# Kernel tuning notes

Measured on AMD Instinct MI355X. Metric: run time of the kernel, lower is better.

## Reference

```python
import jax, jax.numpy as jnp
import numpy as np

NUM_IN = 1024
HIDDEN = 32  # pooling_hidden_dim fixed in PoolingFunction
N = 200000


def setup_inputs() -> dict:
    key = jax.random.key(0)
    ks = jax.random.split(key, 7)
    s_in = 1.0 / np.sqrt(NUM_IN)
    s_h = 1.0 / np.sqrt(HIDDEN)
    return {
        "x": jax.random.normal(ks[0], (N, NUM_IN), dtype=jnp.float32),
        "V_w": jax.random.uniform(ks[1], (HIDDEN, NUM_IN), jnp.float32, -s_in, s_in),
        "V_b": jax.random.uniform(ks[2], (HIDDEN,), jnp.float32, -s_in, s_in),
        "U_w": jax.random.uniform(ks[3], (HIDDEN, NUM_IN), jnp.float32, -s_in, s_in),
        "U_b": jax.random.uniform(ks[4], (HIDDEN,), jnp.float32, -s_in, s_in),
        "w_w": jax.random.uniform(ks[5], (1, HIDDEN), jnp.float32, -s_h, s_h),
        "w_b": jax.random.uniform(ks[6], (1,), jnp.float32, -s_h, s_h),
    }


def reference(x, V_w, V_b, U_w, U_b, w_w, w_b):
    # x: [N, num_in]
    a_v = jnp.tanh(x @ V_w.T + V_b)          # [N, H]
    a_u = jax.nn.sigmoid(x @ U_w.T + U_b)    # [N, H]
    a = (a_v * a_u) @ w_w.T + w_b            # [N, 1] attention logits
    a = jax.nn.softmax(a.T, axis=1)          # [1, N]
    m = a @ x                                # [1, num_in]
    return m
```

## Files before the change

kernel.cpp:

```cpp
#include <hip/hip_runtime.h>
#include <math.h>

#define NUM_IN 1024
#define TILE_R 16
#define NB_MAX 256
#define PR_OSTRIDE 17
#define PR_QSTRIDE (64 * PR_OSTRIDE + 4)

using bf16x8 = __attribute__((ext_vector_type(8))) short;
using f32x4  = __attribute__((ext_vector_type(4))) float;

__device__ __forceinline__ unsigned int f2bf1(float f) {
  unsigned int u = __float_as_uint(f);
  return (u + 0x7fffu + ((u >> 16) & 1u)) >> 16;
}
__device__ __forceinline__ unsigned int pk2(float a, float b) {
  return f2bf1(a) | (f2bf1(b) << 16);
}
__device__ __forceinline__ float bflo(unsigned int w) { return __uint_as_float(w << 16); }
__device__ __forceinline__ float bfhi(unsigned int w) { return __uint_as_float(w & 0xffff0000u); }

#define BARX() do { \
  __builtin_amdgcn_sched_barrier(0); \
  asm volatile("s_waitcnt lgkmcnt(0)" ::: "memory"); \
  __builtin_amdgcn_s_barrier(); \
  __builtin_amdgcn_sched_barrier(0); \
} while (0)

#define WAIT_VM0() do { \
  __builtin_amdgcn_sched_barrier(0); \
  asm volatile("s_waitcnt vmcnt(0)" ::: "memory"); \
  __builtin_amdgcn_sched_barrier(0); \
} while (0)

__global__ __launch_bounds__(512, 1) void ga_main(
    const float* __restrict__ x,
    const float* __restrict__ Vw, const float* __restrict__ Uw,
    const float* __restrict__ Vb, const float* __restrict__ Ub,
    const float* __restrict__ ww, const float* __restrict__ wb,
    float* __restrict__ wsAcc, float* __restrict__ wsM, float* __restrict__ wsS,
    int nb, int nTiles)
{
  __shared__ __align__(16) float prered[8 * PR_QSTRIDE];
  __shared__ __align__(16) float lgs[TILE_R];

  const int tid = threadIdx.x;
  const int b   = blockIdx.x;
  const int w   = tid >> 6;
  const int l   = tid & 63;
  const int l15 = l & 15;
  const int kg  = l >> 4;
  const int h   = tid & 31;
  const int rr  = tid >> 5;

  const float vbh = Vb[h], ubh = Ub[h], wwh = ww[h];
  const float wb0 = wb[0];

  uint4 bfr[4][4];
  {
    #pragma unroll
    for (int nt = 0; nt < 4; ++nt) {
      const int o = (nt << 4) + l15;
      const float* Wr = (o < 32) ? (Vw + (size_t)o * NUM_IN) : (Uw + (size_t)(o - 32) * NUM_IN);
      #pragma unroll
      for (int s = 0; s < 4; ++s) {
        const int k0 = (w << 7) + (s << 5) + (kg << 3);
        const float4 a = *reinterpret_cast<const float4*>(Wr + k0);
        const float4 c = *reinterpret_cast<const float4*>(Wr + k0 + 4);
        uint4 v;
        v.x = pk2(a.x, a.y); v.y = pk2(a.z, a.w);
        v.z = pk2(c.x, c.y); v.w = pk2(c.z, c.w);
        bfr[nt][s] = v;
      }
    }
    #pragma unroll
    for (int nt = 0; nt < 4; ++nt)
      #pragma unroll
      for (int s = 0; s < 4; ++s)
        asm volatile("" : "+v"(bfr[nt][s].x), "+v"(bfr[nt][s].y),
                          "+v"(bfr[nt][s].z), "+v"(bfr[nt][s].w));
  }

  const char* xb8 = (const char*)x;
  const int inRow = (w << 9) + (kg << 5);

  float4 sA[4], sB[4];
  uint4  xf[4];

  #define ISSUE(Tt) do { \
    const char* base_ = xb8 + ((size_t)(Tt) * TILE_R + l15) * 4096 + inRow; \
    sA[0] = *reinterpret_cast<const float4*>(base_      );  sB[0] = *reinterpret_cast<const float4*>(base_ +  16); \
    sA[1] = *reinterpret_cast<const float4*>(base_ + 128);  sB[1] = *reinterpret_cast<const float4*>(base_ + 144); \
    sA[2] = *reinterpret_cast<const float4*>(base_ + 256);  sB[2] = *reinterpret_cast<const float4*>(base_ + 272); \
    sA[3] = *reinterpret_cast<const float4*>(base_ + 384);  sB[3] = *reinterpret_cast<const float4*>(base_ + 400); \
  } while (0)

  #define PACK() do { \
    _Pragma("unroll") \
    for (int s = 0; s < 4; ++s) { \
      xf[s].x = pk2(sA[s].x, sA[s].y); xf[s].y = pk2(sA[s].z, sA[s].w); \
      xf[s].z = pk2(sB[s].x, sB[s].y); xf[s].w = pk2(sB[s].z, sB[s].w); \
    } \
    _Pragma("unroll") \
    for (int s = 0; s < 4; ++s) \
      asm volatile("" : "+v"(xf[s].x), "+v"(xf[s].y), "+v"(xf[s].z), "+v"(xf[s].w)); \
  } while (0)

  float M = -INFINITY, S = 0.f;
  float acc[4][8];
  #pragma unroll
  for (int s = 0; s < 4; ++s)
    #pragma unroll
    for (int i = 0; i < 8; ++i) acc[s][i] = 0.f;

  int T = b;

  ISSUE(T);
  WAIT_VM0();
  PACK();
  if (T + nb < nTiles) ISSUE(T + nb);

  while (true) {
    const bool more1 = (T + nb)     < nTiles;
    const bool more2 = (T + 2 * nb) < nTiles;

    {
      f32x4 a4[4] = {{0.f,0.f,0.f,0.f},{0.f,0.f,0.f,0.f},{0.f,0.f,0.f,0.f},{0.f,0.f,0.f,0.f}};
      #pragma unroll
      for (int s = 0; s < 4; ++s) {
        const bf16x8 af = __builtin_bit_cast(bf16x8, xf[s]);
        #pragma unroll
        for (int nt = 0; nt < 4; ++nt)
          a4[nt] = __builtin_amdgcn_mfma_f32_16x16x32_bf16(
              af, __builtin_bit_cast(bf16x8, bfr[nt][s]), a4[nt], 0, 0, 0);
      }
      #pragma unroll
      for (int nt = 0; nt < 4; ++nt) {
        const int obase = w * PR_QSTRIDE + ((nt << 4) + l15) * PR_OSTRIDE + (kg << 2);
        #pragma unroll
        for (int r = 0; r < 4; ++r) prered[obase + r] = a4[nt][r];
      }
    }
    BARX();

    {
      float pv = vbh, pu = ubh;
      #pragma unroll
      for (int q = 0; q < 8; ++q) {
        pv += prered[q * PR_QSTRIDE + h * PR_OSTRIDE + rr];
        pu += prered[q * PR_QSTRIDE + (h + 32) * PR_OSTRIDE + rr];
      }
      const float ev = __expf(2.f * pv);
      const float av = (ev - 1.f) * __builtin_amdgcn_rcpf(ev + 1.f);
      const float au = __builtin_amdgcn_rcpf(1.f + __expf(-pu));
      float g = av * au * wwh;
      g += __shfl_xor(g, 1);
      g += __shfl_xor(g, 2);
      g += __shfl_xor(g, 4);
      g += __shfl_xor(g, 8);
      g += __shfl_xor(g, 16);
      if (h == 0) lgs[rr] = g + wb0;
    }
    BARX();

    {
      const float lf = lgs[l15];
      float mc = lf;
      mc = fmaxf(mc, __shfl_xor(mc, 1));
      mc = fmaxf(mc, __shfl_xor(mc, 2));
      mc = fmaxf(mc, __shfl_xor(mc, 4));
      mc = fmaxf(mc, __shfl_xor(mc, 8));
      if (mc > M) {
        const float scale = __expf(M - mc);
        S *= scale;
        #pragma unroll
        for (int s = 0; s < 4; ++s)
          #pragma unroll
          for (int i = 0; i < 8; ++i) acc[s][i] *= scale;
        M = mc;
      }
      const float p = __expf(lf - M);
      S += p;
      #pragma unroll
      for (int s = 0; s < 4; ++s) {
        acc[s][0] = fmaf(p, bflo(xf[s].x), acc[s][0]);
        acc[s][1] = fmaf(p, bfhi(xf[s].x), acc[s][1]);
        acc[s][2] = fmaf(p, bflo(xf[s].y), acc[s][2]);
        acc[s][3] = fmaf(p, bfhi(xf[s].y), acc[s][3]);
        acc[s][4] = fmaf(p, bflo(xf[s].z), acc[s][4]);
        acc[s][5] = fmaf(p, bfhi(xf[s].z), acc[s][5]);
        acc[s][6] = fmaf(p, bflo(xf[s].w), acc[s][6]);
        acc[s][7] = fmaf(p, bfhi(xf[s].w), acc[s][7]);
      }
      if (more1) {
        WAIT_VM0();
        PACK();
        if (more2) ISSUE(T + 2 * nb);
      }
    }

    if (!more1) break;
    T += nb;
  }

  #pragma unroll
  for (int d = 1; d < 16; d <<= 1) {
    #pragma unroll
    for (int s = 0; s < 4; ++s)
      #pragma unroll
      for (int i = 0; i < 8; ++i) acc[s][i] += __shfl_xor(acc[s][i], d);
    S += __shfl_xor(S, d);
  }
  if (l15 == 0) {
    #pragma unroll
    for (int s = 0; s < 4; ++s) {
      float* dst = &wsAcc[(size_t)b * NUM_IN + (w << 7) + (s << 5) + (kg << 3)];
      *reinterpret_cast<float4*>(dst)     = make_float4(acc[s][0], acc[s][1], acc[s][2], acc[s][3]);
      *reinterpret_cast<float4*>(dst + 4) = make_float4(acc[s][4], acc[s][5], acc[s][6], acc[s][7]);
    }
  }
  if (tid == 0) { wsM[b] = M; wsS[b] = S; }
}

__global__ void ga_reduceMS(const float* __restrict__ wsM, const float* __restrict__ wsS,
                            float* __restrict__ wsW, float* __restrict__ wsT, int nb)
{
  __shared__ float sm[8], ss[8];
  const int t = threadIdx.x;
  float m = (t < nb) ? wsM[t] : -INFINITY;
  float mm = m;
  #pragma unroll
  for (int d = 1; d < 64; d <<= 1) mm = fmaxf(mm, __shfl_xor(mm, d));
  if ((t & 63) == 0) sm[t >> 6] = mm;
  __syncthreads();
  const float M = fmaxf(fmaxf(fmaxf(sm[0], sm[1]), fmaxf(sm[2], sm[3])),
                        fmaxf(fmaxf(sm[4], sm[5]), fmaxf(sm[6], sm[7])));
  const float wg = (t < nb) ? __expf(m - M) : 0.f;
  if (t < nb) wsW[t] = wg;
  float s = wg * ((t < nb) ? wsS[t] : 0.f);
  #pragma unroll
  for (int d = 1; d < 64; d <<= 1) s += __shfl_xor(s, d);
  if ((t & 63) == 0) ss[t >> 6] = s;
  __syncthreads();
  if (t == 0) {
    float St = 0.f;
    #pragma unroll
    for (int k = 0; k < 8; ++k) St += ss[k];
    wsT[0] = St;
  }
}

__global__ void ga_combine(const float* __restrict__ wsAcc, const float* __restrict__ wsW,
                           const float* __restrict__ wsT, float* __restrict__ out, int nb)
{
  __shared__ float red[8][32];
  const int t = threadIdx.x;
  const int col = (blockIdx.x << 5) + (t & 31);
  const int seg = t >> 5;
  float s = 0.f;
  for (int ii = 0; ii < 64; ++ii) {
    const int i = (seg << 6) + ii;
    if (i < nb) s = fmaf(wsW[i], wsAcc[(size_t)i * NUM_IN + col], s);
  }
  red[seg][t & 31] = s;
  __syncthreads();
  if (seg == 0) {
    float tot = 0.f;
    #pragma unroll
    for (int k = 0; k < 8; ++k) tot += red[k][t];
    out[col] = tot / wsT[0];
  }
}

extern "C" void kernel_launch(void* const* d_in, const int* in_sizes, int n_in,
                              void* d_out, int out_size, void* d_ws, size_t ws_size,
                              hipStream_t stream)
{
  const float* x  = (const float*)d_in[0];
  const float* Vw = (const float*)d_in[1];
  const float* Vb = (const float*)d_in[2];
  const float* Uw = (const float*)d_in[3];
  const float* Ub = (const float*)d_in[4];
  const float* ww = (const float*)d_in[5];
  const float* wb = (const float*)d_in[6];
  float* out = (float*)d_out;

  const int Nrows  = in_sizes[0] / NUM_IN;
  const int nTiles = Nrows / TILE_R;

  const size_t per = (size_t)NUM_IN * 4 + 16;
  int nb = (int)((ws_size - 64) / per);
  if (nb > NB_MAX)  nb = NB_MAX;
  if (nb > nTiles)  nb = nTiles;
  if (nb < 1)       nb = 1;

  float* wsAcc = (float*)d_ws;
  float* wsM   = wsAcc + (size_t)nb * NUM_IN;
  float* wsS   = wsM + nb;
  float* wsW   = wsS + nb;
  float* wsT   = wsW + nb;

  ga_main<<<nb, 512, 0, stream>>>(x, Vw, Uw, Vb, Ub, ww, wb, wsAcc, wsM, wsS, nb, nTiles);
  ga_reduceMS<<<1, 512, 0, stream>>>(wsM, wsS, wsW, wsT, nb);
  ga_combine<<<32, 256, 0, stream>>>(wsAcc, wsW, wsT, out, nb);
}
```

Baseline: 180.5 us.

## Deepen x-tile prefetch to two in-flight loads with double register sets

```diff
diff --git a/kernel.cpp b/kernel.cpp
--- a/kernel.cpp
+++ b/kernel.cpp
@@ -27,9 +27,9 @@
   __builtin_amdgcn_sched_barrier(0); \
 } while (0)
 
-#define WAIT_VM0() do { \
+#define WAIT_VM(n) do { \
   __builtin_amdgcn_sched_barrier(0); \
-  asm volatile("s_waitcnt vmcnt(0)" ::: "memory"); \
+  asm volatile("s_waitcnt vmcnt(" #n ")" ::: "memory"); \
   __builtin_amdgcn_sched_barrier(0); \
 } while (0)
 
@@ -84,22 +84,23 @@
   const char* xb8 = (const char*)x;
   const int inRow = (w << 9) + (kg << 5);
 
-  float4 sA[4], sB[4];
+  float4 sA0[4], sB0[4], sA1[4], sB1[4];
   uint4  xf[4];
 
-  #define ISSUE(Tt) do { \
-    const char* base_ = xb8 + ((size_t)(Tt) * TILE_R + l15) * 4096 + inRow; \
-    sA[0] = *reinterpret_cast<const float4*>(base_      );  sB[0] = *reinterpret_cast<const float4*>(base_ +  16); \
-    sA[1] = *reinterpret_cast<const float4*>(base_ + 128);  sB[1] = *reinterpret_cast<const float4*>(base_ + 144); \
-    sA[2] = *reinterpret_cast<const float4*>(base_ + 256);  sB[2] = *reinterpret_cast<const float4*>(base_ + 272); \
-    sA[3] = *reinterpret_cast<const float4*>(base_ + 384);  sB[3] = *reinterpret_cast<const float4*>(base_ + 400); \
+  #define ISSUE_SET(sa, sb, Tt) do { \
+    const int Tc_ = ((Tt) < nTiles) ? (Tt) : (nTiles - 1); \
+    const char* base_ = xb8 + ((size_t)Tc_ * TILE_R + l15) * 4096 + inRow; \
+    sa[0] = *reinterpret_cast<const float4*>(base_      );  sb[0] = *reinterpret_cast<const float4*>(base_ +  16); \
+    sa[1] = *reinterpret_cast<const float4*>(base_ + 128);  sb[1] = *reinterpret_cast<const float4*>(base_ + 144); \
+    sa[2] = *reinterpret_cast<const float4*>(base_ + 256);  sb[2] = *reinterpret_cast<const float4*>(base_ + 272); \
+    sa[3] = *reinterpret_cast<const float4*>(base_ + 384);  sb[3] = *reinterpret_cast<const float4*>(base_ + 400); \
   } while (0)
 
-  #define PACK() do { \
+  #define PACK_SET(sa, sb) do { \
     _Pragma("unroll") \
     for (int s = 0; s < 4; ++s) { \
-      xf[s].x = pk2(sA[s].x, sA[s].y); xf[s].y = pk2(sA[s].z, sA[s].w); \
-      xf[s].z = pk2(sB[s].x, sB[s].y); xf[s].w = pk2(sB[s].z, sB[s].w); \
+      xf[s].x = pk2(sa[s].x, sa[s].y); xf[s].y = pk2(sa[s].z, sa[s].w); \
+      xf[s].z = pk2(sb[s].x, sb[s].y); xf[s].w = pk2(sb[s].z, sb[s].w); \
     } \
     _Pragma("unroll") \
     for (int s = 0; s < 4; ++s) \
@@ -115,91 +116,95 @@
 
   int T = b;
 
-  ISSUE(T);
-  WAIT_VM0();
-  PACK();
-  if (T + nb < nTiles) ISSUE(T + nb);
+  #define COMPUTE_TILE() do { \
+    { \
+      f32x4 a4[4] = {{0.f,0.f,0.f,0.f},{0.f,0.f,0.f,0.f},{0.f,0.f,0.f,0.f},{0.f,0.f,0.f,0.f}}; \
+      _Pragma("unroll") \
+      for (int s = 0; s < 4; ++s) { \
+        const bf16x8 af = __builtin_bit_cast(bf16x8, xf[s]); \
+        _Pragma("unroll") \
+        for (int nt = 0; nt < 4; ++nt) \
+          a4[nt] = __builtin_amdgcn_mfma_f32_16x16x32_bf16( \
+              af, __builtin_bit_cast(bf16x8, bfr[nt][s]), a4[nt], 0, 0, 0); \
+      } \
+      _Pragma("unroll") \
+      for (int nt = 0; nt < 4; ++nt) { \
+        const int obase = w * PR_QSTRIDE + ((nt << 4) + l15) * PR_OSTRIDE + (kg << 2); \
+        _Pragma("unroll") \
+        for (int r = 0; r < 4; ++r) prered[obase + r] = a4[nt][r]; \
+      } \
+    } \
+    BARX(); \
+    { \
+      float pv = vbh, pu = ubh; \
+      _Pragma("unroll") \
+      for (int q = 0; q < 8; ++q) { \
+        pv += prered[q * PR_QSTRIDE + h * PR_OSTRIDE + rr]; \
+        pu += prered[q * PR_QSTRIDE + (h + 32) * PR_OSTRIDE + rr]; \
+      } \
+      const float ev = __expf(2.f * pv); \
+      const float av = (ev - 1.f) * __builtin_amdgcn_rcpf(ev + 1.f); \
+      const float au = __builtin_amdgcn_rcpf(1.f + __expf(-pu)); \
+      float g = av * au * wwh; \
+      g += __shfl_xor(g, 1); \
+      g += __shfl_xor(g, 2); \
+      g += __shfl_xor(g, 4); \
+      g += __shfl_xor(g, 8); \
+      g += __shfl_xor(g, 16); \
+      if (h == 0) lgs[rr] = g + wb0; \
+    } \
+    BARX(); \
+    { \
+      const float lf = lgs[l15]; \
+      float mc = lf; \
+      mc = fmaxf(mc, __shfl_xor(mc, 1)); \
+      mc = fmaxf(mc, __shfl_xor(mc, 2)); \
+      mc = fmaxf(mc, __shfl_xor(mc, 4)); \
+      mc = fmaxf(mc, __shfl_xor(mc, 8)); \
+      if (mc > M) { \
+        const float scale = __expf(M - mc); \
+        S *= scale; \
+        _Pragma("unroll") \
+        for (int s = 0; s < 4; ++s) \
+          _Pragma("unroll") \
+          for (int i = 0; i < 8; ++i) acc[s][i] *= scale; \
+        M = mc; \
+      } \
+      const float p = __expf(lf - M); \
+      S += p; \
+      _Pragma("unroll") \
+      for (int s = 0; s < 4; ++s) { \
+        acc[s][0] = fmaf(p, bflo(xf[s].x), acc[s][0]); \
+        acc[s][1] = fmaf(p, bfhi(xf[s].x), acc[s][1]); \
+        acc[s][2] = fmaf(p, bflo(xf[s].y), acc[s][2]); \
+        acc[s][3] = fmaf(p, bfhi(xf[s].y), acc[s][3]); \
+        acc[s][4] = fmaf(p, bflo(xf[s].z), acc[s][4]); \
+        acc[s][5] = fmaf(p, bfhi(xf[s].z), acc[s][5]); \
+        acc[s][6] = fmaf(p, bflo(xf[s].w), acc[s][6]); \
+        acc[s][7] = fmaf(p, bfhi(xf[s].w), acc[s][7]); \
+      } \
+    } \
+  } while (0)
+
+  ISSUE_SET(sA0, sB0, T);
+  WAIT_VM(0);
+  PACK_SET(sA0, sB0);
+  ISSUE_SET(sA0, sB0, T + nb);
+  ISSUE_SET(sA1, sB1, T + 2 * nb);
 
   while (true) {
-    const bool more1 = (T + nb)     < nTiles;
-    const bool more2 = (T + 2 * nb) < nTiles;
-
-    {
-      f32x4 a4[4] = {{0.f,0.f,0.f,0.f},{0.f,0.f,0.f,0.f},{0.f,0.f,0.f,0.f},{0.f,0.f,0.f,0.f}};
-      #pragma unroll
-      for (int s = 0; s < 4; ++s) {
-        const bf16x8 af = __builtin_bit_cast(bf16x8, xf[s]);
-        #pragma unroll
-        for (int nt = 0; nt < 4; ++nt)
-          a4[nt] = __builtin_amdgcn_mfma_f32_16x16x32_bf16(
-              af, __builtin_bit_cast(bf16x8, bfr[nt][s]), a4[nt], 0, 0, 0);
-      }
-      #pragma unroll
-      for (int nt = 0; nt < 4; ++nt) {
-        const int obase = w * PR_QSTRIDE + ((nt << 4) + l15) * PR_OSTRIDE + (kg << 2);
-        #pragma unroll
-        for (int r = 0; r < 4; ++r) prered[obase + r] = a4[nt][r];
-      }
-    }
-    BARX();
-
-    {
-      float pv = vbh, pu = ubh;
-      #pragma unroll
-      for (int q = 0; q < 8; ++q) {
-        pv += prered[q * PR_QSTRIDE + h * PR_OSTRIDE + rr];
-        pu += prered[q * PR_QSTRIDE + (h + 32) * PR_OSTRIDE + rr];
-      }
-      const float ev = __expf(2.f * pv);
-      const float av = (ev - 1.f) * __builtin_amdgcn_rcpf(ev + 1.f);
-      const float au = __builtin_amdgcn_rcpf(1.f + __expf(-pu));
-      float g = av * au * wwh;
-      g += __shfl_xor(g, 1);
-      g += __shfl_xor(g, 2);
-      g += __shfl_xor(g, 4);
-      g += __shfl_xor(g, 8);
-      g += __shfl_xor(g, 16);
-      if (h == 0) lgs[rr] = g + wb0;
-    }
-    BARX();
-
-    {
-      const float lf = lgs[l15];
-      float mc = lf;
-      mc = fmaxf(mc, __shfl_xor(mc, 1));
-      mc = fmaxf(mc, __shfl_xor(mc, 2));
-      mc = fmaxf(mc, __shfl_xor(mc, 4));
-      mc = fmaxf(mc, __shfl_xor(mc, 8));
-      if (mc > M) {
-        const float scale = __expf(M - mc);
-        S *= scale;
-        #pragma unroll
-        for (int s = 0; s < 4; ++s)
-          #pragma unroll
-          for (int i = 0; i < 8; ++i) acc[s][i] *= scale;
-        M = mc;
-      }
-      const float p = __expf(lf - M);
-      S += p;
-      #pragma unroll
-      for (int s = 0; s < 4; ++s) {
-        acc[s][0] = fmaf(p, bflo(xf[s].x), acc[s][0]);
-        acc[s][1] = fmaf(p, bfhi(xf[s].x), acc[s][1]);
-        acc[s][2] = fmaf(p, bflo(xf[s].y), acc[s][2]);
-        acc[s][3] = fmaf(p, bfhi(xf[s].y), acc[s][3]);
-        acc[s][4] = fmaf(p, bflo(xf[s].z), acc[s][4]);
-        acc[s][5] = fmaf(p, bfhi(xf[s].z), acc[s][5]);
-        acc[s][6] = fmaf(p, bflo(xf[s].w), acc[s][6]);
-        acc[s][7] = fmaf(p, bfhi(xf[s].w), acc[s][7]);
-      }
-      if (more1) {
-        WAIT_VM0();
-        PACK();
-        if (more2) ISSUE(T + 2 * nb);
-      }
-    }
-
-    if (!more1) break;
+    COMPUTE_TILE();
+    if ((T + nb) >= nTiles) break;
+    WAIT_VM(8);
+    PACK_SET(sA0, sB0);
+    ISSUE_SET(sA0, sB0, T + 3 * nb);
+    T += nb;
+
+    COMPUTE_TILE();
+    if ((T + nb) >= nTiles) break;
+    WAIT_VM(8);
+    PACK_SET(sA1, sB1);
+    ISSUE_SET(sA1, sB1, T + 3 * nb);
     T += nb;
   }
 
```

Result: faster. 174.2 us (-3.5%).
